# Optimization experiments

Measured on AMD Instinct MI355X. Metric: run time of the kernel, lower is better.

## Reference

```python
import jax, jax.numpy as jnp
import numpy as np

H_DIM = 128
C_DIM = 128


def _linear_params(key, in_dim, out_dim):
    kw, kb = jax.random.split(key)
    bound = 1.0 / np.sqrt(in_dim)
    W = jax.random.uniform(kw, (in_dim, out_dim), minval=-bound, maxval=bound, dtype=jnp.float32)
    b = jax.random.uniform(kb, (out_dim,), minval=-bound, maxval=bound, dtype=jnp.float32)
    return W, b


def setup_inputs() -> dict:
    key = jax.random.key(0)
    kx, kh, kc, k1, k2, k3, k4, k5 = jax.random.split(key, 8)
    B = 262144
    x = jax.random.normal(kx, (B, H_DIM), dtype=jnp.float32)
    h = jax.random.normal(kh, (B, H_DIM), dtype=jnp.float32)
    c = jax.random.normal(kc, (B, C_DIM), dtype=jnp.float32)
    Wf, bf = _linear_params(k1, 2 * H_DIM, H_DIM)
    Wi, bi = _linear_params(k2, 2 * H_DIM, H_DIM)
    Wc, bc = _linear_params(k3, 2 * H_DIM, C_DIM)
    Wo, bo = _linear_params(k4, 2 * H_DIM, H_DIM)
    Wch, bch = _linear_params(k5, C_DIM, H_DIM)
    return {"x": x, "h": h, "c": c,
            "Wf": Wf, "bf": bf, "Wi": Wi, "bi": bi,
            "Wc": Wc, "bc": bc, "Wo": Wo, "bo": bo,
            "Wch": Wch, "bch": bch}


def reference(x, h, c, Wf, bf, Wi, bi, Wc, bc, Wo, bo, Wch, bch):
    concat = jnp.concatenate([x, h], axis=-1)  # [B, 2H]
    # Fuse the four gate projections into one GEMM, then split.
    W_gates = jnp.concatenate([Wf, Wi, Wc, Wo], axis=1)  # [2H, 3H+C]
    b_gates = jnp.concatenate([bf, bi, bc, bo], axis=0)
    gates = concat @ W_gates + b_gates
    f_pre, i_pre, ct_pre, o_pre = jnp.split(
        gates, [H_DIM, 2 * H_DIM, 2 * H_DIM + C_DIM], axis=-1)
    f = jax.nn.sigmoid(f_pre)
    i = jax.nn.sigmoid(i_pre)
    c_tilde = jnp.tanh(ct_pre)
    c_new = f * c + i * c_tilde
    o = jax.nn.sigmoid(o_pre)
    h_new = o * jnp.tanh(c_new @ Wch + bch)
    return (h_new, c_new)
```

## Files before the change

kernel.cpp:

```cpp
#include <hip/hip_runtime.h>
#include <hip/hip_bf16.h>


typedef __attribute__((ext_vector_type(8))) short bf16x8;
typedef __attribute__((ext_vector_type(4))) float f32x4;

#define AB0   0
#define AB1   16384
#define LAND0 32768
#define LAND1 65536
#define CLDS0 98304
#define CLDS1 114688
#define CEX0  131072
#define CEX1  139264

static __device__ __forceinline__ unsigned short f2bf(float f) {
    unsigned int u = __builtin_bit_cast(unsigned int, f);
    u += 0x7FFFu + ((u >> 16) & 1u);
    return (unsigned short)(u >> 16);
}

static __device__ __forceinline__ unsigned int cvtpk(float lo, float hi) {
    unsigned int r;
    asm("v_cvt_pk_bf16_f32 %0, %1, %2" : "=v"(r) : "v"(lo), "v"(hi));
    return r;
}

static __device__ __forceinline__ bf16x8 cvt8(f32x4 a, f32x4 b) {
    union { bf16x8 v; unsigned int w[4]; } r;
    r.w[0] = cvtpk(a[0], a[1]);
    r.w[1] = cvtpk(a[2], a[3]);
    r.w[2] = cvtpk(b[0], b[1]);
    r.w[3] = cvtpk(b[2], b[3]);
    return r.v;
}

static __device__ __forceinline__ float fsig(float x) {
    float e = __builtin_amdgcn_exp2f(-1.44269504f * x);
    return __builtin_amdgcn_rcpf(1.0f + e);
}
static __device__ __forceinline__ float ftanh(float x) {
    float e = __builtin_amdgcn_exp2f(2.8853900818f * x);
    return 1.0f - 2.0f * __builtin_amdgcn_rcpf(e + 1.0f);
}

static __device__ __forceinline__ void gload16(const void* gsrc, void* ldst) {
    __builtin_amdgcn_global_load_lds(
        (const __attribute__((address_space(1))) unsigned int*)gsrc,
        (__attribute__((address_space(3))) unsigned int*)ldst,
        16, 0, 0);
}

#define MEMFENCE asm volatile("" ::: "memory")

__global__ void prep_weights(const float* __restrict__ Wf, const float* __restrict__ Wi,
                             const float* __restrict__ Wc, const float* __restrict__ Wo,
                             const float* __restrict__ Wch,
                             unsigned short* __restrict__ WgF,
                             unsigned short* __restrict__ WchF)
{
    int u = blockIdx.x * 256 + threadIdx.x;
    if (u < 16384) {
        int lane = u & 63, g = (u >> 6) & 3, wn = (u >> 8) & 7, ks = u >> 11;
        int l15 = lane & 15, lg = lane >> 4;
        int cg = wn * 16 + l15;
        int k0 = ks * 32 + lg * 8;
        const float* W = (g == 0) ? Wf : (g == 1) ? Wi : (g == 2) ? Wc : Wo;
        union { bf16x8 v; unsigned short s[8]; } r;
#pragma unroll
        for (int i = 0; i < 8; ++i) r.s[i] = f2bf(W[(size_t)(k0 + i) * 128 + cg]);
        *(bf16x8*)(WgF + (size_t)u * 8) = r.v;
    } else if (u < 16384 + 2048) {
        int u2 = u - 16384;
        int lane = u2 & 63, wn = (u2 >> 6) & 7, kt = u2 >> 9;
        int l15 = lane & 15, lg = lane >> 4;
        int col = wn * 16 + l15, k0 = kt * 32 + lg * 8;
        union { bf16x8 v; unsigned short s[8]; } r;
#pragma unroll
        for (int i = 0; i < 8; ++i) r.s[i] = f2bf(Wch[(size_t)(k0 + i) * 128 + col]);
        *(bf16x8*)(WchF + (size_t)u2 * 8) = r.v;
    }
}

#define TILE_BODY(T, CUR)                                                       \
  do {                                                                          \
    const long m0 = base + (long)(T) * 32;                                      \
                                        \
    if ((T) < 31) {                                                             \
      char* cd = lds + ((CUR) ? CLDS0 : CLDS1);                                 \
      gload16(cg + (m0 + 32 + (tid >> 5)) * 128 + (tid & 31) * 4, cd + tid * 16);        \
      gload16(cg + (m0 + 48 + (tid >> 5)) * 128 + (tid & 31) * 4, cd + 8192 + tid * 16); \
    }                                                                           \
    MEMFENCE;                                                                   \
             \
    if ((T) < 31) {                                                             \
      const long ar = ((T) < 30) ? (m0 + 64) : m0;                              \
      char* ad = lds + ((CUR) ? LAND1 : LAND0) + wn * 1024 + lane * 16;         \
      _Pragma("unroll")                                                         \
      for (int j = 0; j < 4; ++j)                                               \
        gload16(dmaA + (ar + wn + j * 8) * 128, ad + j * 8192);                 \
    }                                                                           \
    MEMFENCE;                                                                   \
                           \
    {                                                                           \
      const char* ab = lds + ((CUR) ? AB1 : AB0);                               \
      _Pragma("unroll")                                                         \
      for (int ks = 0; ks < 8; ++ks) {                                          \
        bf16x8 af0 = *(const bf16x8*)(ab + ks * 1024 + ((lane * 16) ^ (ks << 4)));       \
        bf16x8 af1 = *(const bf16x8*)(ab + (8 + ks) * 1024 + ((lane * 16) ^ (ks << 4))); \
        _Pragma("unroll")                                                       \
        for (int g_ = 0; g_ < 4; ++g_) {                                        \
          acc[0][g_] = __builtin_amdgcn_mfma_f32_16x16x32_bf16(af0, Breg[ks][g_], acc[0][g_], 0, 0, 0); \
          acc[1][g_] = __builtin_amdgcn_mfma_f32_16x16x32_bf16(af1, Breg[ks][g_], acc[1][g_], 0, 0, 0); \
        }                                                                       \
      }                                                                         \
    }                                                                           \
                \
    {                                                                           \
      char* cexb = lds + ((CUR) ? CEX1 : CEX0);                                 \
      const char* cbr = lds + ((CUR) ? CLDS1 : CLDS0);                          \
      _Pragma("unroll")                                                         \
      for (int am = 0; am < 2; ++am)                                            \
        _Pragma("unroll")                                                       \
        for (int r = 0; r < 4; ++r) {                                           \
          float cval = *(const float*)(cbr + (am * 16 + lg * 4 + r) * 512 + colc * 4); \
          float f_  = fsig(acc[am][0][r] + bfb);                                \
          float i_  = fsig(acc[am][1][r] + bib);                                \
          float ct_ = ftanh(acc[am][2][r] + bcb);                               \
          float cv_ = f_ * cval + i_ * ct_;                                     \
          coutp[(m0 + am * 16 + lg * 4 + r) * 128 + colc] = cv_;                \
          *(unsigned short*)(cexb + (am * 4 + (wn >> 1)) * 1024                 \
               + (cslotbase + lg * 4 + r) * 16 + (l15 & 7) * 2) = f2bf(cv_);    \
        }                                                                       \
    }                                                                           \
    MEMFENCE;                                                                   \
     \
    if ((T) < 31) {                                                             \
      asm volatile("s_waitcnt vmcnt(22)" ::: "memory");                         \
      const char* ln = lds + ((CUR) ? LAND0 : LAND1) + rowA * 1024;             \
      f32x4 q0 = *(const f32x4*)(ln + (((kgA * 4 + 0) ^ swzA) << 4));           \
      f32x4 q1 = *(const f32x4*)(ln + (((kgA * 4 + 1) ^ swzA) << 4));           \
      f32x4 q2 = *(const f32x4*)(ln + (((kgA * 4 + 2) ^ swzA) << 4));           \
      f32x4 q3 = *(const f32x4*)(ln + (((kgA * 4 + 3) ^ swzA) << 4));           \
      char* fb = lds + ((CUR) ? AB0 : AB1);                                     \
      *(bf16x8*)(fb + aoff0) = cvt8(q0, q1);                                    \
      *(bf16x8*)(fb + aoff1) = cvt8(q2, q3);                                    \
    }                                                                           \
    \
    asm volatile("s_waitcnt lgkmcnt(0) vmcnt(12)" ::: "memory");                \
    __builtin_amdgcn_s_barrier();                                               \
    __builtin_amdgcn_sched_barrier(0);                                          \
                                     \
    {                                                                           \
      const char* cexr = lds + ((CUR) ? CEX1 : CEX0);                           \
      f32x4 acc2_0 = {0.f,0.f,0.f,0.f}, acc2_1 = {0.f,0.f,0.f,0.f};             \
      _Pragma("unroll")                                                         \
      for (int kt = 0; kt < 4; ++kt) {                                          \
        bf16x8 p0 = *(const bf16x8*)(cexr + kt * 1024 + lane * 16);             \
        bf16x8 p1 = *(const bf16x8*)(cexr + (4 + kt) * 1024 + lane * 16);       \
        acc2_0 = __builtin_amdgcn_mfma_f32_16x16x32_bf16(p0, Wreg[kt], acc2_0, 0, 0, 0); \
        acc2_1 = __builtin_amdgcn_mfma_f32_16x16x32_bf16(p1, Wreg[kt], acc2_1, 0, 0, 0); \
      }                                                                         \
      _Pragma("unroll")                                                         \
      for (int r = 0; r < 4; ++r) {                                             \
        float o0 = fsig(acc[0][3][r] + bob);                                    \
        houtp[(m0 +      lg * 4 + r) * 128 + colc] = o0 * ftanh(acc2_0[r] + bchb); \
        float o1 = fsig(acc[1][3][r] + bob);                                    \
        houtp[(m0 + 16 + lg * 4 + r) * 128 + colc] = o1 * ftanh(acc2_1[r] + bchb); \
      }                                                                         \
    }                                                                           \
    _Pragma("unroll")                                                           \
    for (int am = 0; am < 2; ++am)                                              \
      _Pragma("unroll")                                                         \
      for (int g_ = 0; g_ < 4; ++g_) acc[am][g_] = (f32x4){0.f,0.f,0.f,0.f};    \
  } while (0)

__global__ __launch_bounds__(512, 2) void lstm_fused(
    const float* __restrict__ xg, const float* __restrict__ hg, const float* __restrict__ cg,
    const float* __restrict__ bfv, const float* __restrict__ biv,
    const float* __restrict__ bcv, const float* __restrict__ bov,
    const float* __restrict__ bchv,
    const unsigned short* __restrict__ WgF, const unsigned short* __restrict__ WchF,
    float* __restrict__ out, int nrows)
{
    __shared__ uint4 lds4[9216];
    char* lds = (char*)lds4;

    const int tid  = threadIdx.x;
    const int lane = tid & 63;
    const int wn   = tid >> 6;
    const int l15  = lane & 15;
    const int lg   = lane >> 4;
    const long base = (long)blockIdx.x << 10;

    float* houtp = out;
    float* coutp = out + (size_t)nrows * 128;

    const int colc = wn * 16 + l15;
    const float bfb = bfv[colc], bib = biv[colc], bcb = bcv[colc],
                bob = bov[colc], bchb = bchv[colc];
    const int cslotbase = ((wn & 1) * 2 + (l15 >> 3)) * 16;

    bf16x8 Breg[8][4];
#pragma unroll
    for (int ks = 0; ks < 8; ++ks)
#pragma unroll
        for (int g = 0; g < 4; ++g)
            Breg[ks][g] = *(const bf16x8*)(WgF + (size_t)((ks * 32 + wn * 4 + g) * 512 + lane * 8));
    bf16x8 Wreg[4];
#pragma unroll
    for (int kt = 0; kt < 4; ++kt)
        Wreg[kt] = *(const bf16x8*)(WchF + (size_t)((kt * 8 + wn) * 512 + lane * 8));

    const int gu = lane ^ wn;
    const float* dmaA = ((gu < 32) ? (xg + gu * 4) : (hg + (gu - 32) * 4));

    const int rowA = tid >> 4;
    const int kgA  = tid & 15;
    const int swzA = rowA & 7;
    const int ksA  = kgA >> 1;
    const int lgA  = (kgA & 1) * 2;
    const int amA  = rowA >> 4;
    const int l15A = rowA & 15;
    const int aoff0 = (amA * 8 + ksA) * 1024 + ((((lgA    ) * 16 + l15A) * 16) ^ (ksA << 4));
    const int aoff1 = (amA * 8 + ksA) * 1024 + ((((lgA + 1) * 16 + l15A) * 16) ^ (ksA << 4));
    const float* asrc = (kgA < 8) ? (xg + kgA * 16) : (hg + (kgA - 8) * 16);

    gload16(cg + (base + (tid >> 5)) * 128 + (tid & 31) * 4, lds + CLDS0 + tid * 16);
    gload16(cg + (base + 16 + (tid >> 5)) * 128 + (tid & 31) * 4, lds + CLDS0 + 8192 + tid * 16);
    MEMFENCE;
    {
        char* ad = lds + LAND1 + wn * 1024 + lane * 16;
#pragma unroll
        for (int j = 0; j < 4; ++j)
            gload16(dmaA + (base + 32 + wn + j * 8) * 128, ad + j * 8192);
    }
    MEMFENCE;
    {
        const float* s = asrc + (base + rowA) * 128;
        f32x4 v0 = ((const f32x4*)s)[0], v1 = ((const f32x4*)s)[1],
              v2 = ((const f32x4*)s)[2], v3 = ((const f32x4*)s)[3];
        *(bf16x8*)(lds + AB0 + aoff0) = cvt8(v0, v1);
        *(bf16x8*)(lds + AB0 + aoff1) = cvt8(v2, v3);
    }
    asm volatile("s_waitcnt lgkmcnt(0) vmcnt(0)" ::: "memory");
    __builtin_amdgcn_s_barrier();

    f32x4 acc[2][4];
#pragma unroll
    for (int am = 0; am < 2; ++am)
#pragma unroll
        for (int g = 0; g < 4; ++g) acc[am][g] = {0.f, 0.f, 0.f, 0.f};

#pragma unroll 1
    for (int t = 0; t < 32; t += 2) {
        TILE_BODY(t,     0);
        TILE_BODY(t + 1, 1);
    }
}

extern "C" void kernel_launch(void* const* d_in, const int* in_sizes, int n_in,
                              void* d_out, int out_size, void* d_ws, size_t ws_size,
                              hipStream_t stream)
{
    const float* x   = (const float*)d_in[0];
    const float* h   = (const float*)d_in[1];
    const float* c   = (const float*)d_in[2];
    const float* Wf  = (const float*)d_in[3];
    const float* bf_ = (const float*)d_in[4];
    const float* Wi  = (const float*)d_in[5];
    const float* bi_ = (const float*)d_in[6];
    const float* Wc  = (const float*)d_in[7];
    const float* bc_ = (const float*)d_in[8];
    const float* Wo  = (const float*)d_in[9];
    const float* bo_ = (const float*)d_in[10];
    const float* Wch = (const float*)d_in[11];
    const float* bch = (const float*)d_in[12];

    unsigned short* WgF  = (unsigned short*)d_ws;
    unsigned short* WchF = WgF + 512 * 256;
    float* out = (float*)d_out;

    int nrows = in_sizes[0] / 128;

    prep_weights<<<dim3(72), dim3(256), 0, stream>>>(Wf, Wi, Wc, Wo, Wch, WgF, WchF);
    lstm_fused<<<dim3(nrows / 1024), dim3(512), 0, stream>>>(
        x, h, c, bf_, bi_, bc_, bo_, bch, WgF, WchF, out, nrows);
}
```

Before: 144.7 us.

## Defer second GEMM and h output by one tile to drop a barrier per tile

The c_new@Wch MFMA and the h_new output for tile T are moved into the body of tile T+1. This removes the second barrier-separated phase within each tile. The o-gate sigmoid is now computed early and carried across tiles as packed bf16 in registers, with prologue and epilogue tiles peeled. The goal is one barrier per tile and overlap of the small GEMM with the gate epilogue. The cost is more live registers, reduced precision on the o gate, and retuned vmcnt waits that could be wrong.

```diff
diff --git a/kernel.cpp b/kernel.cpp
--- a/kernel.cpp
+++ b/kernel.cpp
@@ -33,6 +33,13 @@
     r.w[2] = cvtpk(b[0], b[1]);
     r.w[3] = cvtpk(b[2], b[3]);
     return r.v;
+}
+
+static __device__ __forceinline__ float obf_lo(unsigned int u) {
+    return __builtin_bit_cast(float, u << 16);
+}
+static __device__ __forceinline__ float obf_hi(unsigned int u) {
+    return __builtin_bit_cast(float, u & 0xFFFF0000u);
 }
 
 static __device__ __forceinline__ float fsig(float x) {
@@ -82,7 +89,7 @@
     }
 }
 
-#define TILE_BODY(T, CUR)                                                       \
+#define TILE_BODY(T, CUR, OKIN, OKOUT, VMC, HP)                                 \
   do {                                                                          \
     const long m0 = base + (long)(T) * 32;                                      \
                                         \
@@ -92,7 +99,7 @@
       gload16(cg + (m0 + 48 + (tid >> 5)) * 128 + (tid & 31) * 4, cd + 8192 + tid * 16); \
     }                                                                           \
     MEMFENCE;                                                                   \
-             \
+      \
     if ((T) < 31) {                                                             \
       const long ar = ((T) < 30) ? (m0 + 64) : m0;                              \
       char* ad = lds + ((CUR) ? LAND1 : LAND0) + wn * 1024 + lane * 16;         \
@@ -101,7 +108,7 @@
         gload16(dmaA + (ar + wn + j * 8) * 128, ad + j * 8192);                 \
     }                                                                           \
     MEMFENCE;                                                                   \
-                           \
+                        \
     {                                                                           \
       const char* ab = lds + ((CUR) ? AB1 : AB0);                               \
       _Pragma("unroll")                                                         \
@@ -115,28 +122,56 @@
         }                                                                       \
       }                                                                         \
     }                                                                           \
-                \
+        \
     {                                                                           \
-      char* cexb = lds + ((CUR) ? CEX1 : CEX0);                                 \
-      const char* cbr = lds + ((CUR) ? CLDS1 : CLDS0);                          \
-      _Pragma("unroll")                                                         \
-      for (int am = 0; am < 2; ++am)                                            \
+      f32x4 acc2_0 = {0.f,0.f,0.f,0.f}, acc2_1 = {0.f,0.f,0.f,0.f};             \
+      if (HP) {                                                                 \
+        const char* cexr = lds + ((CUR) ? CEX0 : CEX1);                         \
+        _Pragma("unroll")                                                       \
+        for (int kt = 0; kt < 4; ++kt) {                                        \
+          bf16x8 p0 = *(const bf16x8*)(cexr + kt * 1024 + lane * 16);           \
+          bf16x8 p1 = *(const bf16x8*)(cexr + (4 + kt) * 1024 + lane * 16);     \
+          acc2_0 = __builtin_amdgcn_mfma_f32_16x16x32_bf16(p0, Wreg[kt], acc2_0, 0, 0, 0); \
+          acc2_1 = __builtin_amdgcn_mfma_f32_16x16x32_bf16(p1, Wreg[kt], acc2_1, 0, 0, 0); \
+        }                                                                       \
+      }                                                                         \
+       \
+      {                                                                         \
+        char* cexb = lds + ((CUR) ? CEX1 : CEX0);                               \
+        const char* cbr = lds + ((CUR) ? CLDS1 : CLDS0);                        \
+        _Pragma("unroll")                                                       \
+        for (int am = 0; am < 2; ++am) {                                        \
+          float ov[4];                                                          \
+          _Pragma("unroll")                                                     \
+          for (int r = 0; r < 4; ++r) {                                         \
+            float cval = *(const float*)(cbr + (am * 16 + lg * 4 + r) * 512 + colc * 4); \
+            float f_  = fsig(acc[am][0][r] + bfb);                              \
+            float i_  = fsig(acc[am][1][r] + bib);                              \
+            float ct_ = ftanh(acc[am][2][r] + bcb);                             \
+            float cv_ = f_ * cval + i_ * ct_;                                   \
+            ov[r] = fsig(acc[am][3][r] + bob);                                  \
+            coutp[(m0 + am * 16 + lg * 4 + r) * 128 + colc] = cv_;              \
+            *(unsigned short*)(cexb + (am * 4 + (wn >> 1)) * 1024               \
+                 + (cslotbase + lg * 4 + r) * 16 + (l15 & 7) * 2) = f2bf(cv_);  \
+          }                                                                     \
+          OKOUT[am][0] = (unsigned int)f2bf(ov[0]) | ((unsigned int)f2bf(ov[1]) << 16); \
+          OKOUT[am][1] = (unsigned int)f2bf(ov[2]) | ((unsigned int)f2bf(ov[3]) << 16); \
+        }                                                                       \
+      }                                                                         \
+                                                           \
+      if (HP) {                                                                 \
         _Pragma("unroll")                                                       \
         for (int r = 0; r < 4; ++r) {                                           \
-          float cval = *(const float*)(cbr + (am * 16 + lg * 4 + r) * 512 + colc * 4); \
-          float f_  = fsig(acc[am][0][r] + bfb);                                \
-          float i_  = fsig(acc[am][1][r] + bib);                                \
-          float ct_ = ftanh(acc[am][2][r] + bcb);                               \
-          float cv_ = f_ * cval + i_ * ct_;                                     \
-          coutp[(m0 + am * 16 + lg * 4 + r) * 128 + colc] = cv_;                \
-          *(unsigned short*)(cexb + (am * 4 + (wn >> 1)) * 1024                 \
-               + (cslotbase + lg * 4 + r) * 16 + (l15 & 7) * 2) = f2bf(cv_);    \
+          float o0 = (r & 1) ? obf_hi(OKIN[0][r >> 1]) : obf_lo(OKIN[0][r >> 1]); \
+          float o1 = (r & 1) ? obf_hi(OKIN[1][r >> 1]) : obf_lo(OKIN[1][r >> 1]); \
+          houtp[(m0 - 32 +      lg * 4 + r) * 128 + colc] = o0 * ftanh(acc2_0[r] + bchb); \
+          houtp[(m0 - 32 + 16 + lg * 4 + r) * 128 + colc] = o1 * ftanh(acc2_1[r] + bchb); \
         }                                                                       \
+      }                                                                         \
     }                                                                           \
     MEMFENCE;                                                                   \
      \
     if ((T) < 31) {                                                             \
-      asm volatile("s_waitcnt vmcnt(22)" ::: "memory");                         \
       const char* ln = lds + ((CUR) ? LAND0 : LAND1) + rowA * 1024;             \
       f32x4 q0 = *(const f32x4*)(ln + (((kgA * 4 + 0) ^ swzA) << 4));           \
       f32x4 q1 = *(const f32x4*)(ln + (((kgA * 4 + 1) ^ swzA) << 4));           \
@@ -146,29 +181,11 @@
       *(bf16x8*)(fb + aoff0) = cvt8(q0, q1);                                    \
       *(bf16x8*)(fb + aoff1) = cvt8(q2, q3);                                    \
     }                                                                           \
-    \
-    asm volatile("s_waitcnt lgkmcnt(0) vmcnt(12)" ::: "memory");                \
+                                   \
+    asm volatile("s_waitcnt lgkmcnt(0) vmcnt(" #VMC ")" ::: "memory");          \
+    __builtin_amdgcn_sched_barrier(0);                                          \
     __builtin_amdgcn_s_barrier();                                               \
     __builtin_amdgcn_sched_barrier(0);                                          \
-                                     \
-    {                                                                           \
-      const char* cexr = lds + ((CUR) ? CEX1 : CEX0);                           \
-      f32x4 acc2_0 = {0.f,0.f,0.f,0.f}, acc2_1 = {0.f,0.f,0.f,0.f};             \
-      _Pragma("unroll")                                                         \
-      for (int kt = 0; kt < 4; ++kt) {                                          \
-        bf16x8 p0 = *(const bf16x8*)(cexr + kt * 1024 + lane * 16);             \
-        bf16x8 p1 = *(const bf16x8*)(cexr + (4 + kt) * 1024 + lane * 16);       \
-        acc2_0 = __builtin_amdgcn_mfma_f32_16x16x32_bf16(p0, Wreg[kt], acc2_0, 0, 0, 0); \
-        acc2_1 = __builtin_amdgcn_mfma_f32_16x16x32_bf16(p1, Wreg[kt], acc2_1, 0, 0, 0); \
-      }                                                                         \
-      _Pragma("unroll")                                                         \
-      for (int r = 0; r < 4; ++r) {                                             \
-        float o0 = fsig(acc[0][3][r] + bob);                                    \
-        houtp[(m0 +      lg * 4 + r) * 128 + colc] = o0 * ftanh(acc2_0[r] + bchb); \
-        float o1 = fsig(acc[1][3][r] + bob);                                    \
-        houtp[(m0 + 16 + lg * 4 + r) * 128 + colc] = o1 * ftanh(acc2_1[r] + bchb); \
-      }                                                                         \
-    }                                                                           \
     _Pragma("unroll")                                                           \
     for (int am = 0; am < 2; ++am)                                              \
       _Pragma("unroll")                                                         \
@@ -244,7 +261,9 @@
         *(bf16x8*)(lds + AB0 + aoff1) = cvt8(v2, v3);
     }
     asm volatile("s_waitcnt lgkmcnt(0) vmcnt(0)" ::: "memory");
+    __builtin_amdgcn_sched_barrier(0);
     __builtin_amdgcn_s_barrier();
+    __builtin_amdgcn_sched_barrier(0);
 
     f32x4 acc[2][4];
 #pragma unroll
@@ -252,10 +271,38 @@
 #pragma unroll
         for (int g = 0; g < 4; ++g) acc[am][g] = {0.f, 0.f, 0.f, 0.f};
 
+    unsigned int ok0[2][2], ok1[2][2];
+    ok0[0][0] = ok0[0][1] = ok0[1][0] = ok0[1][1] = 0;
+    ok1[0][0] = ok1[0][1] = ok1[1][0] = ok1[1][1] = 0;
+
+    TILE_BODY(0, 0, ok1, ok0, 8, 0);
+
 #pragma unroll 1
-    for (int t = 0; t < 32; t += 2) {
-        TILE_BODY(t,     0);
-        TILE_BODY(t + 1, 1);
+    for (int t = 1; t < 31; t += 2) {
+        TILE_BODY(t,     1, ok0, ok1, 16, 1);
+        TILE_BODY(t + 1, 0, ok1, ok0, 16, 1);
+    }
+
+    TILE_BODY(31, 1, ok0, ok1, 16, 1);
+
+    {
+        const char* cexr = lds + CEX1;
+        f32x4 acc2_0 = {0.f,0.f,0.f,0.f}, acc2_1 = {0.f,0.f,0.f,0.f};
+#pragma unroll
+        for (int kt = 0; kt < 4; ++kt) {
+            bf16x8 p0 = *(const bf16x8*)(cexr + kt * 1024 + lane * 16);
+            bf16x8 p1 = *(const bf16x8*)(cexr + (4 + kt) * 1024 + lane * 16);
+            acc2_0 = __builtin_amdgcn_mfma_f32_16x16x32_bf16(p0, Wreg[kt], acc2_0, 0, 0, 0);
+            acc2_1 = __builtin_amdgcn_mfma_f32_16x16x32_bf16(p1, Wreg[kt], acc2_1, 0, 0, 0);
+        }
+        const long mL = base + 31 * 32;
+#pragma unroll
+        for (int r = 0; r < 4; ++r) {
+            float o0 = (r & 1) ? obf_hi(ok1[0][r >> 1]) : obf_lo(ok1[0][r >> 1]);
+            float o1 = (r & 1) ? obf_hi(ok1[1][r >> 1]) : obf_lo(ok1[1][r >> 1]);
+            houtp[(mL +      lg * 4 + r) * 128 + colc] = o0 * ftanh(acc2_0[r] + bchb);
+            houtp[(mL + 16 + lg * 4 + r) * 128 + colc] = o1 * ftanh(acc2_1[r] + bchb);
+        }
     }
 }
 
```

New measurement: 252.4 us. 74.5% more time.
